# Kernel tuning notes

Hardware: AMD Instinct MI355X
Metric: run time of the kernel (lower is better)

## Reference

```python
import jax, jax.numpy as jnp
import numpy as np

B, N, D, H, DK, DV, R = 4, 256, 256, 8, 32, 32, 64
EPS = 1e-6


def setup_inputs() -> dict:
    key = jax.random.key(0)
    ks = jax.random.split(key, 16)
    s = D ** -0.5
    return {
        "q": jax.random.normal(ks[0], (B, N, D), jnp.float32),
        "k": jax.random.normal(ks[1], (B, N, D), jnp.float32),
        "v": jax.random.normal(ks[2], (B, N, D), jnp.float32),
        "mask": jax.random.randint(ks[3], (B, N, N), 0, 2).astype(jnp.int32),
        "link": jax.random.uniform(ks[4], (B, N, N, R), jnp.float32),
        "Wq": jax.random.normal(ks[5], (D, H * DK), jnp.float32) * s,
        "Wk": jax.random.normal(ks[6], (D, H * DK), jnp.float32) * s,
        "Wr": jax.random.normal(ks[7], (D, H * DK), jnp.float32) * s,
        "Wv": jax.random.normal(ks[8], (D, H * DV), jnp.float32) * s,
        "Wvv": jax.random.normal(ks[9], (D, H * DV), jnp.float32) * s,
        "relationE": jax.random.normal(ks[10], (R, D), jnp.float32) * s,
        "Wo": jax.random.normal(ks[11], (H * DV, D), jnp.float32) * s,
        "gamma": jnp.ones((D,), jnp.float32),
        "beta": jnp.zeros((D,), jnp.float32),
    }


def reference(q, k, v, mask, link, Wq, Wk, Wr, Wv, Wvv, relationE, Wo, gamma, beta):
    # rela_num != 0 branch of Ruleformer MultiHeadAttention (dropout = identity, eval mode).
    residual = q
    b, n, d = q.shape
    # per-head projections of X (== q == residual in this branch): [b,h,n,dk]
    Xq = (q @ Wq).reshape(b, n, H, DK).transpose(0, 2, 1, 3)
    Xk = (q @ Wk).reshape(b, n, H, DK).transpose(0, 2, 1, 3)
    Xv = (q @ Wv).reshape(b, n, H, DV).transpose(0, 2, 1, 3)

    # calcE: relation-biased scores. Rk[b,i,j,h,d] = (link @ relationE @ Wr)
    Rk = jnp.einsum('bijr,re->bije', link, relationE @ Wr).reshape(b, n, n, H, DK)
    # attn[b,h,i,j] = Xq[b,h,i] . (Xk[b,h,j] + Rk[b,i,j,h])
    attn = jnp.einsum('bhid,bhjd->bhij', Xq, Xk)
    attn = attn + jnp.einsum('bijhd,bhid->bhij', Rk, Xq)
    attn = attn / (DK ** 0.5)
    attn = jnp.where(mask[:, None, :, :] == 0, -1e9, attn)
    alpha = jax.nn.softmax(attn, axis=-1)  # [b,h,n,n]

    # calcZ: Z[b,h,i] = sum_j alpha[b,h,i,j] * (Xv[b,h,j] + Rv[b,i,j,h])
    Rv = jnp.einsum('bijr,re->bije', link, relationE @ Wvv).reshape(b, n, n, H, DV)
    Z = jnp.einsum('bhij,bhjd->bhid', alpha, Xv)
    Z = Z + jnp.einsum('bhij,bijhd->bhid', alpha, Rv)

    out = Z.transpose(0, 2, 1, 3).reshape(b, n, H * DV) @ Wo
    out = out + residual
    mu = out.mean(-1, keepdims=True)
    var = ((out - mu) ** 2).mean(-1, keepdims=True)
    out = (out - mu) * jax.lax.rsqrt(var + EPS) * gamma + beta
    return out, alpha
```

## Files before the change

### kernel.cpp

```cpp
#include <hip/hip_runtime.h>
#include <math.h>

constexpr int B_ = 4, N_ = 256, D_ = 256, H_ = 8, DK_ = 32, DV_ = 32, R_ = 64;
constexpr float SCALE_ = 0.17677669529663687f;
constexpr float EPS_ = 1e-6f;

__global__ __launch_bounds__(256) void ekev_kernel(
        const float* __restrict__ relE, const float* __restrict__ Wr,
        const float* __restrict__ Wvv, float* __restrict__ Ek,
        float* __restrict__ Ev) {
    int r = blockIdx.x & 63;
    int which = blockIdx.x >> 6;
    const float* W = which ? Wvv : Wr;
    float* out = which ? Ev : Ek;
    __shared__ float row[256];
    int tid = threadIdx.x;
    row[tid] = relE[r * 256 + tid];
    __syncthreads();
    float acc = 0.f;
    for (int d = 0; d < 256; ++d) acc += row[d] * W[d * 256 + tid];
    out[r * 256 + tid] = acc;
}

__global__ __launch_bounds__(256) void mcat_kernel(
        const float* __restrict__ Wq, const float* __restrict__ Ek,
        float* __restrict__ M) {
    int d = blockIdx.x;
    int t = threadIdx.x;
    __shared__ float wrow[256];
    wrow[t] = Wq[d * 256 + t];
    __syncthreads();
    for (int hr = t; hr < 512; hr += 256) {
        int h = hr >> 6, r = hr & 63;
        const float4* ek4 = (const float4*)(Ek + r * 256 + h * 32);
        const float4* w4 = (const float4*)(wrow + h * 32);
        float acc = 0.f;
#pragma unroll
        for (int k = 0; k < 8; ++k) {
            float4 e = ek4[k], w = w4[k];
            acc += e.x * w.x + e.y * w.y + e.z * w.z + e.w * w.w;
        }
        M[d * 512 + hr] = acc;
    }
}

__global__ __launch_bounds__(256) void projT_kernel(
        const float* __restrict__ q, const float* __restrict__ Wq,
        const float* __restrict__ Wk, const float* __restrict__ Wv,
        const float* __restrict__ M, float* __restrict__ Xq,
        float* __restrict__ Xk, float* __restrict__ Xv,
        float* __restrict__ T) {
    int rt = blockIdx.x / 20, ct = blockIdx.x % 20;
    int t = threadIdx.x;
    __shared__ float qsh[32 * 256];
    {
        const float4* qb = (const float4*)(q + rt * 32 * 256);
        float4* qs = (float4*)qsh;
#pragma unroll
        for (int k = 0; k < 8; ++k) qs[t + k * 256] = qb[t + k * 256];
    }
    __syncthreads();
    int c = t & 63, rg = t >> 6;
    const float* W;
    int ncols, ccol;
    if (ct < 4)       { W = Wq; ccol = ct * 64 + c;        ncols = 256; }
    else if (ct < 8)  { W = Wk; ccol = (ct - 4) * 64 + c;  ncols = 256; }
    else if (ct < 12) { W = Wv; ccol = (ct - 8) * 64 + c;  ncols = 256; }
    else              { W = M;  ccol = (ct - 12) * 64 + c; ncols = 512; }
    float acc[8] = {0.f, 0.f, 0.f, 0.f, 0.f, 0.f, 0.f, 0.f};
    for (int d4 = 0; d4 < 64; ++d4) {
        float w0 = W[(d4 * 4 + 0) * ncols + ccol];
        float w1 = W[(d4 * 4 + 1) * ncols + ccol];
        float w2 = W[(d4 * 4 + 2) * ncols + ccol];
        float w3 = W[(d4 * 4 + 3) * ncols + ccol];
#pragma unroll
        for (int ii = 0; ii < 8; ++ii) {
            float4 qv = *(const float4*)(qsh + (rg * 8 + ii) * 256 + d4 * 4);
            acc[ii] += qv.x * w0 + qv.y * w1 + qv.z * w2 + qv.w * w3;
        }
    }
#pragma unroll
    for (int ii = 0; ii < 8; ++ii) {
        int row = rt * 32 + rg * 8 + ii;
        int b = row >> 8, n = row & 255;
        if (ct < 12) {
            int h = ccol >> 5, dk = ccol & 31;
            float* dst = (ct < 4) ? Xq : (ct < 8) ? Xk : Xv;
            dst[((b * 8 + h) * 256 + n) * 32 + dk] = acc[ii];
        } else {
            T[(size_t)row * 512 + ccol] = acc[ii];
        }
    }
}

__global__ __launch_bounds__(256) void qk_kernel(
        const float* __restrict__ Xq, const float* __restrict__ Xk,
        float* __restrict__ qk) {
    int x = blockIdx.x;
    int jt = x & 3, it = (x >> 2) & 3, bh = x >> 4;
    int t = threadIdx.x;
    __shared__ float xqsh[32 * 64];
    __shared__ float xksh[32 * 64];
#pragma unroll
    for (int k = 0; k < 2; ++k) {
        int m = t + k * 256;
        int i = m >> 3, dq4 = m & 7;
        float4 v = *(const float4*)(Xq + ((size_t)(bh * 256 + it * 64 + i)) * 32 + dq4 * 4);
        xqsh[(dq4 * 4 + 0) * 64 + i] = v.x;
        xqsh[(dq4 * 4 + 1) * 64 + i] = v.y;
        xqsh[(dq4 * 4 + 2) * 64 + i] = v.z;
        xqsh[(dq4 * 4 + 3) * 64 + i] = v.w;
        float4 u = *(const float4*)(Xk + ((size_t)(bh * 256 + jt * 64 + i)) * 32 + dq4 * 4);
        xksh[(dq4 * 4 + 0) * 64 + i] = u.x;
        xksh[(dq4 * 4 + 1) * 64 + i] = u.y;
        xksh[(dq4 * 4 + 2) * 64 + i] = u.z;
        xksh[(dq4 * 4 + 3) * 64 + i] = u.w;
    }
    __syncthreads();
    int ti = t >> 4, tj = t & 15;
    float acc[4][4];
#pragma unroll
    for (int a = 0; a < 4; ++a)
#pragma unroll
        for (int bb = 0; bb < 4; ++bb) acc[a][bb] = 0.f;
    for (int dk = 0; dk < 32; ++dk) {
        float xa0 = xqsh[dk * 64 + ti * 4 + 0];
        float xa1 = xqsh[dk * 64 + ti * 4 + 1];
        float xa2 = xqsh[dk * 64 + ti * 4 + 2];
        float xa3 = xqsh[dk * 64 + ti * 4 + 3];
        float xb0 = xksh[dk * 64 + tj * 4 + 0];
        float xb1 = xksh[dk * 64 + tj * 4 + 1];
        float xb2 = xksh[dk * 64 + tj * 4 + 2];
        float xb3 = xksh[dk * 64 + tj * 4 + 3];
        acc[0][0] += xa0 * xb0; acc[0][1] += xa0 * xb1; acc[0][2] += xa0 * xb2; acc[0][3] += xa0 * xb3;
        acc[1][0] += xa1 * xb0; acc[1][1] += xa1 * xb1; acc[1][2] += xa1 * xb2; acc[1][3] += xa1 * xb3;
        acc[2][0] += xa2 * xb0; acc[2][1] += xa2 * xb1; acc[2][2] += xa2 * xb2; acc[2][3] += xa2 * xb3;
        acc[3][0] += xa3 * xb0; acc[3][1] += xa3 * xb1; acc[3][2] += xa3 * xb2; acc[3][3] += xa3 * xb3;
    }
#pragma unroll
    for (int a = 0; a < 4; ++a) {
        int i = it * 64 + ti * 4 + a;
        float4 v = make_float4(acc[a][0], acc[a][1], acc[a][2], acc[a][3]);
        *(float4*)(qk + ((size_t)(bh * 256 + i)) * 256 + jt * 64 + tj * 4) = v;
    }
}

__global__ __launch_bounds__(256) void bias_kernel(
        const float* __restrict__ link, const float* __restrict__ T,
        float* __restrict__ biasOut) {
    int x = blockIdx.x;
    int jt = x & 3, bi = x >> 2;
    int b = bi >> 8, i = bi & 255;
    int t = threadIdx.x;
    __shared__ float linksh[64 * 67];
    __shared__ float Tsh[512];
    __shared__ float part[4 * 512];
    Tsh[t] = T[(size_t)bi * 512 + t];
    Tsh[256 + t] = T[(size_t)bi * 512 + 256 + t];
    {
        const float4* lp = (const float4*)(link + ((size_t)(bi * 256 + jt * 64)) * 64);
#pragma unroll
        for (int k = 0; k < 4; ++k) {
            int m = t + k * 256;
            float4 v = lp[m];
            int j = m >> 4, c = (m & 15) * 4;
            float* dst = linksh + j * 67 + c;
            dst[0] = v.x; dst[1] = v.y; dst[2] = v.z; dst[3] = v.w;
        }
    }
    __syncthreads();
    int j = t & 63, rg = t >> 6;
    float pacc[8] = {0.f, 0.f, 0.f, 0.f, 0.f, 0.f, 0.f, 0.f};
    for (int rr = 0; rr < 16; ++rr) {
        int r = rg * 16 + rr;
        float lv = linksh[j * 67 + r];
#pragma unroll
        for (int h = 0; h < 8; ++h) pacc[h] += lv * Tsh[h * 64 + r];
    }
#pragma unroll
    for (int h = 0; h < 8; ++h) part[rg * 512 + h * 64 + j] = pacc[h];
    __syncthreads();
    int hp = t >> 6;
#pragma unroll
    for (int e = 0; e < 2; ++e) {
        int h = hp * 2 + e;
        float sum = part[h * 64 + j] + part[512 + h * 64 + j] +
                    part[1024 + h * 64 + j] + part[1536 + h * 64 + j];
        biasOut[((size_t)(b * 8 + h) * 256 + i) * 256 + jt * 64 + j] = sum;
    }
}

__global__ __launch_bounds__(256) void softmax_kernel(
        const float* __restrict__ qk, const int* __restrict__ mask,
        float* __restrict__ alpha) {
    int bi = blockIdx.x;
    int b = bi >> 8, i = bi & 255;
    int t = threadIdx.x;
    __shared__ float redsh[64];
    int j = t;
    float s[8];
#pragma unroll
    for (int h = 0; h < 8; ++h) {
        size_t off = ((size_t)(b * 8 + h) * 256 + i) * 256 + j;
        s[h] = (qk[((size_t)(b * 8 + h) * 256 + i) * 256 + j] + alpha[off]) * SCALE_;
    }
    if (mask[(b * 256 + i) * 256 + j] == 0) {
#pragma unroll
        for (int h = 0; h < 8; ++h) s[h] = -1e9f;
    }
    int lane = t & 63, wv = t >> 6;
#pragma unroll
    for (int h = 0; h < 8; ++h) {
        float v = s[h];
        for (int off = 32; off > 0; off >>= 1) v = fmaxf(v, __shfl_xor(v, off));
        if (lane == 0) redsh[h * 4 + wv] = v;
    }
    __syncthreads();
    float mx[8];
#pragma unroll
    for (int h = 0; h < 8; ++h)
        mx[h] = fmaxf(fmaxf(redsh[h * 4 + 0], redsh[h * 4 + 1]),
                      fmaxf(redsh[h * 4 + 2], redsh[h * 4 + 3]));
    __syncthreads();
#pragma unroll
    for (int h = 0; h < 8; ++h) {
        float e = __expf(s[h] - mx[h]);
        s[h] = e;
        float v = e;
        for (int off = 32; off > 0; off >>= 1) v += __shfl_xor(v, off);
        if (lane == 0) redsh[h * 4 + wv] = v;
    }
    __syncthreads();
#pragma unroll
    for (int h = 0; h < 8; ++h) {
        float esum = redsh[h * 4 + 0] + redsh[h * 4 + 1] +
                     redsh[h * 4 + 2] + redsh[h * 4 + 3];
        alpha[((size_t)(b * 8 + h) * 256 + i) * 256 + j] = s[h] * (1.f / esum);
    }
}

__global__ __launch_bounds__(256) void spart_kernel(
        const float* __restrict__ link, const float* __restrict__ alpha,
        float* __restrict__ Spart) {
    int x = blockIdx.x;
    int jt = x & 1, bi = x >> 1;
    int b = bi >> 8, i = bi & 255;
    int t = threadIdx.x;
    __shared__ float linksh[128 * 67];
    __shared__ float ash[1024];
    __shared__ float part[4 * 512];
    {
        const float4* lp = (const float4*)(link + ((size_t)(bi * 256 + jt * 128)) * 64);
#pragma unroll
        for (int k = 0; k < 8; ++k) {
            int m = t + k * 256;
            float4 v = lp[m];
            int j = m >> 4, c = (m & 15) * 4;
            float* dst = linksh + j * 67 + c;
            dst[0] = v.x; dst[1] = v.y; dst[2] = v.z; dst[3] = v.w;
        }
    }
#pragma unroll
    for (int k = 0; k < 4; ++k) {
        int m = t + k * 256;
        int h = m >> 7, j = m & 127;
        ash[m] = alpha[((size_t)(b * 8 + h) * 256 + i) * 256 + jt * 128 + j];
    }
    __syncthreads();
    int r = t & 63, jg = t >> 6;
    float pacc[8] = {0.f, 0.f, 0.f, 0.f, 0.f, 0.f, 0.f, 0.f};
    for (int jj = 0; jj < 32; ++jj) {
        int j = jg * 32 + jj;
        float lv = linksh[j * 67 + r];
#pragma unroll
        for (int h = 0; h < 8; ++h) pacc[h] += ash[h * 128 + j] * lv;
    }
#pragma unroll
    for (int h = 0; h < 8; ++h) part[jg * 512 + h * 64 + r] = pacc[h];
    __syncthreads();
    for (int hr = t; hr < 512; hr += 256) {
        float sum = part[hr] + part[512 + hr] + part[1024 + hr] + part[1536 + hr];
        Spart[(size_t)x * 512 + hr] = sum;
    }
}

__global__ __launch_bounds__(256) void zx_kernel(
        const float* __restrict__ alpha, const float* __restrict__ Xv,
        float* __restrict__ Zx) {
    int x = blockIdx.x;
    int it = x & 7, bh = x >> 3;
    int t = threadIdx.x;
    __shared__ float ash[32 * 64];
    __shared__ float xvsh[64 * 32];
    int dv = t & 31, ig = t >> 5;
    float acc[4] = {0.f, 0.f, 0.f, 0.f};
    for (int cc = 0; cc < 4; ++cc) {
        __syncthreads();
#pragma unroll
        for (int k = 0; k < 2; ++k) {
            int m = t + k * 256;
            int i = m >> 4, jq = m & 15;
            float4 v = *(const float4*)(alpha + ((size_t)(bh * 256 + it * 32 + i)) * 256 + cc * 64 + jq * 4);
            float* dst = ash + i * 64 + jq * 4;
            dst[0] = v.x; dst[1] = v.y; dst[2] = v.z; dst[3] = v.w;
            ((float4*)xvsh)[m] = *(const float4*)(Xv + ((size_t)(bh * 256 + cc * 64)) * 32 + m * 4);
        }
        __syncthreads();
        for (int j = 0; j < 64; ++j) {
            float xv = xvsh[j * 32 + dv];
#pragma unroll
            for (int ii = 0; ii < 4; ++ii)
                acc[ii] += ash[(ig * 4 + ii) * 64 + j] * xv;
        }
    }
#pragma unroll
    for (int ii = 0; ii < 4; ++ii)
        Zx[((size_t)(bh * 256 + it * 32 + ig * 4 + ii)) * 32 + dv] = acc[ii];
}

__global__ __launch_bounds__(256) void outz_kernel(
        const float* __restrict__ Spart, const float* __restrict__ Zx,
        const float* __restrict__ Ev, const float* __restrict__ Wo,
        const float* __restrict__ q, const float* __restrict__ gamma,
        const float* __restrict__ beta, float* __restrict__ out) {
    int blk = blockIdx.x;
    int t = threadIdx.x;
    __shared__ float Ssh[4 * 512];
    __shared__ float zsh[4 * 256];
    __shared__ float redsh[32];
    for (int m = t; m < 2048; m += 256) {
        int rr = m >> 9, hr = m & 511;
        size_t bi = (size_t)(blk * 4 + rr);
        Ssh[m] = Spart[bi * 1024 + hr] + Spart[bi * 1024 + 512 + hr];
    }
    __syncthreads();
    int h = t >> 5, dv = t & 31;
    int row0 = blk * 4;
    int b = row0 >> 8;
    float z[4];
#pragma unroll
    for (int rr = 0; rr < 4; ++rr) {
        int i = (row0 + rr) & 255;
        z[rr] = Zx[((size_t)((b * 8 + h) * 256 + i)) * 32 + dv];
    }
    for (int r = 0; r < 64; ++r) {
        float ev = Ev[r * 256 + h * 32 + dv];
#pragma unroll
        for (int rr = 0; rr < 4; ++rr) z[rr] += Ssh[rr * 512 + h * 64 + r] * ev;
    }
#pragma unroll
    for (int rr = 0; rr < 4; ++rr) zsh[rr * 256 + t] = z[rr];
    __syncthreads();
    float acc[4];
#pragma unroll
    for (int rr = 0; rr < 4; ++rr) acc[rr] = q[(row0 + rr) * 256 + t];
    for (int d4 = 0; d4 < 64; ++d4) {
        float w0 = Wo[(d4 * 4 + 0) * 256 + t];
        float w1 = Wo[(d4 * 4 + 1) * 256 + t];
        float w2 = Wo[(d4 * 4 + 2) * 256 + t];
        float w3 = Wo[(d4 * 4 + 3) * 256 + t];
#pragma unroll
        for (int rr = 0; rr < 4; ++rr) {
            float4 zv = *(const float4*)(zsh + rr * 256 + d4 * 4);
            acc[rr] += zv.x * w0 + zv.y * w1 + zv.z * w2 + zv.w * w3;
        }
    }
    int lane = t & 63, wv = t >> 6;
#pragma unroll
    for (int rr = 0; rr < 4; ++rr) {
        float v = acc[rr], v2 = acc[rr] * acc[rr];
        for (int off = 32; off > 0; off >>= 1) {
            v += __shfl_xor(v, off);
            v2 += __shfl_xor(v2, off);
        }
        if (lane == 0) {
            redsh[rr * 8 + wv] = v;
            redsh[rr * 8 + 4 + wv] = v2;
        }
    }
    __syncthreads();
#pragma unroll
    for (int rr = 0; rr < 4; ++rr) {
        float sum = redsh[rr * 8 + 0] + redsh[rr * 8 + 1] + redsh[rr * 8 + 2] + redsh[rr * 8 + 3];
        float sum2 = redsh[rr * 8 + 4] + redsh[rr * 8 + 5] + redsh[rr * 8 + 6] + redsh[rr * 8 + 7];
        float mu = sum * (1.f / 256.f);
        float var = sum2 * (1.f / 256.f) - mu * mu;
        float dev = acc[rr] - mu;
        out[(row0 + rr) * 256 + t] = dev * rsqrtf(var + EPS_) * gamma[t] + beta[t];
    }
}

extern "C" void kernel_launch(void* const* d_in, const int* in_sizes, int n_in,
                              void* d_out, int out_size, void* d_ws, size_t ws_size,
                              hipStream_t stream) {
    const float* q     = (const float*)d_in[0];
    const int*   mask  = (const int*)d_in[3];
    const float* link  = (const float*)d_in[4];
    const float* Wq    = (const float*)d_in[5];
    const float* Wk    = (const float*)d_in[6];
    const float* Wr    = (const float*)d_in[7];
    const float* Wv    = (const float*)d_in[8];
    const float* Wvv   = (const float*)d_in[9];
    const float* relE  = (const float*)d_in[10];
    const float* Wo    = (const float*)d_in[11];
    const float* gamma = (const float*)d_in[12];
    const float* beta  = (const float*)d_in[13];

    float* out   = (float*)d_out;
    float* alpha = out + B_ * N_ * D_;

    float* ws    = (float*)d_ws;
    float* Ek    = ws;
    float* Ev    = Ek + 16384;
    float* Mcat  = Ev + 16384;
    float* Xq    = Mcat + 131072;
    float* Xk    = Xq + 262144;
    float* Xv    = Xk + 262144;
    float* T     = Xv + 262144;
    float* qkbuf = T + 524288;
    float* Spart = qkbuf + 2097152;
    float* Zx    = Spart + 1048576;

    ekev_kernel<<<128, 256, 0, stream>>>(relE, Wr, Wvv, Ek, Ev);
    mcat_kernel<<<256, 256, 0, stream>>>(Wq, Ek, Mcat);
    projT_kernel<<<640, 256, 0, stream>>>(q, Wq, Wk, Wv, Mcat, Xq, Xk, Xv, T);
    qk_kernel<<<512, 256, 0, stream>>>(Xq, Xk, qkbuf);
    bias_kernel<<<4096, 256, 0, stream>>>(link, T, alpha);
    softmax_kernel<<<1024, 256, 0, stream>>>(qkbuf, mask, alpha);
    spart_kernel<<<2048, 256, 0, stream>>>(link, alpha, Spart);
    zx_kernel<<<256, 256, 0, stream>>>(alpha, Xv, Zx);
    outz_kernel<<<256, 256, 0, stream>>>(Spart, Zx, Ev, Wo, q, gamma, beta, out);
}
```

Measured before the change: 229.5 us.

## Fuse QK dot product into softmax and retile projection as 64x64 register-blocked GEMM

Removes the separate qk kernel and its 8MB intermediate buffer by computing the Xq·Xk dot products inside the softmax kernel, where each thread reads its own Xk row for each head. The projection kernel is restructured from a row-tile sweep into a K-chunked 64x64 shared-memory tiled GEMM with 4x4 register blocking and float4 stores. This cuts a kernel launch and a large write-read round trip, at the cost of redundant Xk reads across the 256 rows i in softmax, where each thread reads a strided 128-byte row.

```diff
diff --git a/kernel.cpp b/kernel.cpp
--- a/kernel.cpp
+++ b/kernel.cpp
@@ -50,98 +50,72 @@
         const float* __restrict__ M, float* __restrict__ Xq,
         float* __restrict__ Xk, float* __restrict__ Xv,
         float* __restrict__ T) {
-    int rt = blockIdx.x / 20, ct = blockIdx.x % 20;
-    int t = threadIdx.x;
-    __shared__ float qsh[32 * 256];
-    {
-        const float4* qb = (const float4*)(q + rt * 32 * 256);
-        float4* qs = (float4*)qsh;
-#pragma unroll
-        for (int k = 0; k < 8; ++k) qs[t + k * 256] = qb[t + k * 256];
-    }
-    __syncthreads();
-    int c = t & 63, rg = t >> 6;
+    int ct = blockIdx.x >> 4, rt = blockIdx.x & 15;
+    int t = threadIdx.x;
+    __shared__ float ash[32 * 65];
+    __shared__ float bsh[32 * 64];
     const float* W;
-    int ncols, ccol;
-    if (ct < 4)       { W = Wq; ccol = ct * 64 + c;        ncols = 256; }
-    else if (ct < 8)  { W = Wk; ccol = (ct - 4) * 64 + c;  ncols = 256; }
-    else if (ct < 12) { W = Wv; ccol = (ct - 8) * 64 + c;  ncols = 256; }
-    else              { W = M;  ccol = (ct - 12) * 64 + c; ncols = 512; }
-    float acc[8] = {0.f, 0.f, 0.f, 0.f, 0.f, 0.f, 0.f, 0.f};
-    for (int d4 = 0; d4 < 64; ++d4) {
-        float w0 = W[(d4 * 4 + 0) * ncols + ccol];
-        float w1 = W[(d4 * 4 + 1) * ncols + ccol];
-        float w2 = W[(d4 * 4 + 2) * ncols + ccol];
-        float w3 = W[(d4 * 4 + 3) * ncols + ccol];
-#pragma unroll
-        for (int ii = 0; ii < 8; ++ii) {
-            float4 qv = *(const float4*)(qsh + (rg * 8 + ii) * 256 + d4 * 4);
-            acc[ii] += qv.x * w0 + qv.y * w1 + qv.z * w2 + qv.w * w3;
-        }
-    }
-#pragma unroll
-    for (int ii = 0; ii < 8; ++ii) {
-        int row = rt * 32 + rg * 8 + ii;
-        int b = row >> 8, n = row & 255;
-        if (ct < 12) {
-            int h = ccol >> 5, dk = ccol & 31;
-            float* dst = (ct < 4) ? Xq : (ct < 8) ? Xk : Xv;
-            dst[((b * 8 + h) * 256 + n) * 32 + dk] = acc[ii];
-        } else {
-            T[(size_t)row * 512 + ccol] = acc[ii];
-        }
-    }
-}
-
-__global__ __launch_bounds__(256) void qk_kernel(
-        const float* __restrict__ Xq, const float* __restrict__ Xk,
-        float* __restrict__ qk) {
-    int x = blockIdx.x;
-    int jt = x & 3, it = (x >> 2) & 3, bh = x >> 4;
-    int t = threadIdx.x;
-    __shared__ float xqsh[32 * 64];
-    __shared__ float xksh[32 * 64];
-#pragma unroll
-    for (int k = 0; k < 2; ++k) {
-        int m = t + k * 256;
-        int i = m >> 3, dq4 = m & 7;
-        float4 v = *(const float4*)(Xq + ((size_t)(bh * 256 + it * 64 + i)) * 32 + dq4 * 4);
-        xqsh[(dq4 * 4 + 0) * 64 + i] = v.x;
-        xqsh[(dq4 * 4 + 1) * 64 + i] = v.y;
-        xqsh[(dq4 * 4 + 2) * 64 + i] = v.z;
-        xqsh[(dq4 * 4 + 3) * 64 + i] = v.w;
-        float4 u = *(const float4*)(Xk + ((size_t)(bh * 256 + jt * 64 + i)) * 32 + dq4 * 4);
-        xksh[(dq4 * 4 + 0) * 64 + i] = u.x;
-        xksh[(dq4 * 4 + 1) * 64 + i] = u.y;
-        xksh[(dq4 * 4 + 2) * 64 + i] = u.z;
-        xksh[(dq4 * 4 + 3) * 64 + i] = u.w;
-    }
-    __syncthreads();
+    int ncols, cbase;
+    if (ct < 4)       { W = Wq; cbase = ct * 64;        ncols = 256; }
+    else if (ct < 8)  { W = Wk; cbase = (ct - 4) * 64;  ncols = 256; }
+    else if (ct < 12) { W = Wv; cbase = (ct - 8) * 64;  ncols = 256; }
+    else              { W = M;  cbase = (ct - 12) * 64; ncols = 512; }
     int ti = t >> 4, tj = t & 15;
-    float acc[4][4];
-#pragma unroll
-    for (int a = 0; a < 4; ++a)
-#pragma unroll
-        for (int bb = 0; bb < 4; ++bb) acc[a][bb] = 0.f;
-    for (int dk = 0; dk < 32; ++dk) {
-        float xa0 = xqsh[dk * 64 + ti * 4 + 0];
-        float xa1 = xqsh[dk * 64 + ti * 4 + 1];
-        float xa2 = xqsh[dk * 64 + ti * 4 + 2];
-        float xa3 = xqsh[dk * 64 + ti * 4 + 3];
-        float xb0 = xksh[dk * 64 + tj * 4 + 0];
-        float xb1 = xksh[dk * 64 + tj * 4 + 1];
-        float xb2 = xksh[dk * 64 + tj * 4 + 2];
-        float xb3 = xksh[dk * 64 + tj * 4 + 3];
-        acc[0][0] += xa0 * xb0; acc[0][1] += xa0 * xb1; acc[0][2] += xa0 * xb2; acc[0][3] += xa0 * xb3;
-        acc[1][0] += xa1 * xb0; acc[1][1] += xa1 * xb1; acc[1][2] += xa1 * xb2; acc[1][3] += xa1 * xb3;
-        acc[2][0] += xa2 * xb0; acc[2][1] += xa2 * xb1; acc[2][2] += xa2 * xb2; acc[2][3] += xa2 * xb3;
-        acc[3][0] += xa3 * xb0; acc[3][1] += xa3 * xb1; acc[3][2] += xa3 * xb2; acc[3][3] += xa3 * xb3;
-    }
-#pragma unroll
-    for (int a = 0; a < 4; ++a) {
-        int i = it * 64 + ti * 4 + a;
-        float4 v = make_float4(acc[a][0], acc[a][1], acc[a][2], acc[a][3]);
-        *(float4*)(qk + ((size_t)(bh * 256 + i)) * 256 + jt * 64 + tj * 4) = v;
+    float acc[4][4] = {{0.f}};
+    for (int kc = 0; kc < 8; ++kc) {
+        __syncthreads();
+#pragma unroll
+        for (int kk = 0; kk < 2; ++kk) {
+            int m = t + kk * 256;
+            int i = m >> 3, kq = m & 7;
+            float4 v = *(const float4*)(q + (size_t)(rt * 64 + i) * 256 + kc * 32 + kq * 4);
+            ash[(kq * 4 + 0) * 65 + i] = v.x;
+            ash[(kq * 4 + 1) * 65 + i] = v.y;
+            ash[(kq * 4 + 2) * 65 + i] = v.z;
+            ash[(kq * 4 + 3) * 65 + i] = v.w;
+        }
+#pragma unroll
+        for (int kk = 0; kk < 2; ++kk) {
+            int m = t + kk * 256;
+            int k = m >> 4, j4 = m & 15;
+            float4 v = *(const float4*)(W + (size_t)(kc * 32 + k) * ncols + cbase + j4 * 4);
+            *(float4*)(bsh + k * 64 + j4 * 4) = v;
+        }
+        __syncthreads();
+#pragma unroll 8
+        for (int k = 0; k < 32; ++k) {
+            float4 av = *(const float4*)(ash + k * 65 + ti * 4);
+            float4 bv = *(const float4*)(bsh + k * 64 + tj * 4);
+            acc[0][0] += av.x * bv.x; acc[0][1] += av.x * bv.y;
+            acc[0][2] += av.x * bv.z; acc[0][3] += av.x * bv.w;
+            acc[1][0] += av.y * bv.x; acc[1][1] += av.y * bv.y;
+            acc[1][2] += av.y * bv.z; acc[1][3] += av.y * bv.w;
+            acc[2][0] += av.z * bv.x; acc[2][1] += av.z * bv.y;
+            acc[2][2] += av.z * bv.z; acc[2][3] += av.z * bv.w;
+            acc[3][0] += av.w * bv.x; acc[3][1] += av.w * bv.y;
+            acc[3][2] += av.w * bv.z; acc[3][3] += av.w * bv.w;
+        }
+    }
+    if (ct < 12) {
+        float* dst = (ct < 4) ? Xq : (ct < 8) ? Xv : Xv;
+        dst = (ct < 4) ? Xq : (ct < 8) ? Xk : Xv;
+        int gcol = (ct & 3) * 64 + tj * 4;
+        int h = gcol >> 5, dk = gcol & 31;
+#pragma unroll
+        for (int a = 0; a < 4; ++a) {
+            int row = rt * 64 + ti * 4 + a;
+            int bb = row >> 8, n = row & 255;
+            *(float4*)(dst + ((size_t)(bb * 8 + h) * 256 + n) * 32 + dk) =
+                make_float4(acc[a][0], acc[a][1], acc[a][2], acc[a][3]);
+        }
+    } else {
+        int gcol = (ct - 12) * 64 + tj * 4;
+#pragma unroll
+        for (int a = 0; a < 4; ++a) {
+            int row = rt * 64 + ti * 4 + a;
+            *(float4*)(T + (size_t)row * 512 + gcol) =
+                make_float4(acc[a][0], acc[a][1], acc[a][2], acc[a][3]);
+        }
     }
 }
 
@@ -190,19 +164,32 @@
     }
 }
 
-__global__ __launch_bounds__(256) void softmax_kernel(
-        const float* __restrict__ qk, const int* __restrict__ mask,
-        float* __restrict__ alpha) {
+__global__ __launch_bounds__(256) void qksoftmax_kernel(
+        const float* __restrict__ Xq, const float* __restrict__ Xk,
+        const int* __restrict__ mask, float* __restrict__ alpha) {
     int bi = blockIdx.x;
     int b = bi >> 8, i = bi & 255;
     int t = threadIdx.x;
+    __shared__ float Xqsh[256];
     __shared__ float redsh[64];
+    {
+        int h = t >> 5, d = t & 31;
+        Xqsh[t] = Xq[((b * 8 + h) * 256 + i) * 32 + d];
+    }
+    __syncthreads();
     int j = t;
     float s[8];
 #pragma unroll
     for (int h = 0; h < 8; ++h) {
-        size_t off = ((size_t)(b * 8 + h) * 256 + i) * 256 + j;
-        s[h] = (qk[((size_t)(b * 8 + h) * 256 + i) * 256 + j] + alpha[off]) * SCALE_;
+        const float4* xk4 = (const float4*)(Xk + ((size_t)((b * 8 + h) * 256 + j)) * 32);
+        const float4* xq4 = (const float4*)(Xqsh + h * 32);
+        float d = 0.f;
+#pragma unroll
+        for (int d4 = 0; d4 < 8; ++d4) {
+            float4 a = xk4[d4], c = xq4[d4];
+            d += a.x * c.x + a.y * c.y + a.z * c.z + a.w * c.w;
+        }
+        s[h] = (d + alpha[((size_t)(b * 8 + h) * 256 + i) * 256 + j]) * SCALE_;
     }
     if (mask[(b * 256 + i) * 256 + j] == 0) {
 #pragma unroll
@@ -247,7 +234,7 @@
     int b = bi >> 8, i = bi & 255;
     int t = threadIdx.x;
     __shared__ float linksh[128 * 67];
-    __shared__ float ash[1024];
+    __shared__ float ashm[1024];
     __shared__ float part[4 * 512];
     {
         const float4* lp = (const float4*)(link + ((size_t)(bi * 256 + jt * 128)) * 64);
@@ -264,7 +251,7 @@
     for (int k = 0; k < 4; ++k) {
         int m = t + k * 256;
         int h = m >> 7, j = m & 127;
-        ash[m] = alpha[((size_t)(b * 8 + h) * 256 + i) * 256 + jt * 128 + j];
+        ashm[m] = alpha[((size_t)(b * 8 + h) * 256 + i) * 256 + jt * 128 + j];
     }
     __syncthreads();
     int r = t & 63, jg = t >> 6;
@@ -273,7 +260,7 @@
         int j = jg * 32 + jj;
         float lv = linksh[j * 67 + r];
 #pragma unroll
-        for (int h = 0; h < 8; ++h) pacc[h] += ash[h * 128 + j] * lv;
+        for (int h = 0; h < 8; ++h) pacc[h] += ashm[h * 128 + j] * lv;
     }
 #pragma unroll
     for (int h = 0; h < 8; ++h) part[jg * 512 + h * 64 + r] = pacc[h];
@@ -290,7 +277,7 @@
     int x = blockIdx.x;
     int it = x & 7, bh = x >> 3;
     int t = threadIdx.x;
-    __shared__ float ash[32 * 64];
+    __shared__ float ashm[32 * 64];
     __shared__ float xvsh[64 * 32];
     int dv = t & 31, ig = t >> 5;
     float acc[4] = {0.f, 0.f, 0.f, 0.f};
@@ -301,7 +288,7 @@
             int m = t + k * 256;
             int i = m >> 4, jq = m & 15;
             float4 v = *(const float4*)(alpha + ((size_t)(bh * 256 + it * 32 + i)) * 256 + cc * 64 + jq * 4);
-            float* dst = ash + i * 64 + jq * 4;
+            float* dst = ashm + i * 64 + jq * 4;
             dst[0] = v.x; dst[1] = v.y; dst[2] = v.z; dst[3] = v.w;
             ((float4*)xvsh)[m] = *(const float4*)(Xv + ((size_t)(bh * 256 + cc * 64)) * 32 + m * 4);
         }
@@ -310,7 +297,7 @@
             float xv = xvsh[j * 32 + dv];
 #pragma unroll
             for (int ii = 0; ii < 4; ++ii)
-                acc[ii] += ash[(ig * 4 + ii) * 64 + j] * xv;
+                acc[ii] += ashm[(ig * 4 + ii) * 64 + j] * xv;
         }
     }
 #pragma unroll
@@ -417,16 +404,14 @@
     float* Xk    = Xq + 262144;
     float* Xv    = Xk + 262144;
     float* T     = Xv + 262144;
-    float* qkbuf = T + 524288;
-    float* Spart = qkbuf + 2097152;
+    float* Spart = T + 524288;
     float* Zx    = Spart + 1048576;
 
     ekev_kernel<<<128, 256, 0, stream>>>(relE, Wr, Wvv, Ek, Ev);
     mcat_kernel<<<256, 256, 0, stream>>>(Wq, Ek, Mcat);
-    projT_kernel<<<640, 256, 0, stream>>>(q, Wq, Wk, Wv, Mcat, Xq, Xk, Xv, T);
-    qk_kernel<<<512, 256, 0, stream>>>(Xq, Xk, qkbuf);
+    projT_kernel<<<320, 256, 0, stream>>>(q, Wq, Wk, Wv, Mcat, Xq, Xk, Xv, T);
     bias_kernel<<<4096, 256, 0, stream>>>(link, T, alpha);
-    softmax_kernel<<<1024, 256, 0, stream>>>(qkbuf, mask, alpha);
+    qksoftmax_kernel<<<1024, 256, 0, stream>>>(Xq, Xk, mask, alpha);
     spart_kernel<<<2048, 256, 0, stream>>>(link, alpha, Spart);
     zx_kernel<<<256, 256, 0, stream>>>(alpha, Xv, Zx);
     outz_kernel<<<256, 256, 0, stream>>>(Spart, Zx, Ev, Wo, q, gamma, beta, out);
```

Measured after the change: 231.1 us. No clear change (+0.7%).
